# Performance work log

Hardware: AMD Instinct MI355X
Metric: run time of the kernel (lower is better)

## Reference

```python
import jax, jax.numpy as jnp
import numpy as np

B, L, D, H, HS, V, NL = 8, 513, 512, 8, 64, 513, 6  # head_size = D // H
EPS = 1e-5


def setup_inputs() -> dict:
    key = jax.random.key(0)
    ks = jax.random.split(key, 8)
    s = 0.02
    return {
        "x": jax.random.randint(ks[0], (B, L), 0, V),
        "embed": jax.random.normal(ks[1], (V, D), jnp.float32) * s,
        "pos_embed": jax.random.normal(ks[2], (L, D), jnp.float32) * s,
        "Wq": jax.random.normal(ks[3], (NL, H, D, HS), jnp.float32) * s,
        "Wk": jax.random.normal(ks[4], (NL, H, D, HS), jnp.float32) * s,
        "Wv": jax.random.normal(ks[5], (NL, H, D, HS), jnp.float32) * s,
        "ln1_g": jnp.ones((NL, D), jnp.float32),
        "ln1_b": jnp.zeros((NL, D), jnp.float32),
        "ln2_g": jnp.ones((NL, D), jnp.float32),
        "ln2_b": jnp.zeros((NL, D), jnp.float32),
        "mlp_W": jax.random.normal(ks[6], (NL, D, D), jnp.float32) * s,
        "mlp_b": jnp.zeros((NL, D), jnp.float32),
        "fc_W": jax.random.normal(ks[7], (D, V), jnp.float32) * s,
        "fc_b": jnp.zeros((V,), jnp.float32),
    }


def _layernorm(x, g, b):
    mu = jnp.mean(x, axis=-1, keepdims=True)
    var = jnp.mean(jnp.square(x - mu), axis=-1, keepdims=True)
    return (x - mu) * jax.lax.rsqrt(var + EPS) * g + b


def reference(x, embed, pos_embed, Wq, Wk, Wv, ln1_g, ln1_b, ln2_g, ln2_b,
              mlp_W, mlp_b, fc_W, fc_b):
    h = embed[x] + pos_embed[None]                       # (B, L, D)
    mask = jnp.tril(jnp.ones((L, L), bool))              # causal tril buffer
    scale = HS ** -0.5
    for i in range(NL):
        xn = _layernorm(h, ln1_g[i], ln1_b[i])
        # all heads batched (original loops per head; same math)
        q = jnp.einsum('bld,hde->bhle', xn, Wq[i])
        k = jnp.einsum('bld,hde->bhle', xn, Wk[i])
        v = jnp.einsum('bld,hde->bhle', xn, Wv[i])
        w = jnp.einsum('bhle,bhme->bhlm', q, k) * scale
        w = jnp.where(mask, w, -jnp.inf)
        w = jax.nn.softmax(w, axis=-1)
        y = jnp.einsum('bhlm,bhme->bhle', w, v)
        y = y.transpose(0, 2, 1, 3).reshape(B, L, D)     # concat heads
        h = y + h
        xn2 = _layernorm(h, ln2_g[i], ln2_b[i])
        h = jax.nn.gelu(xn2 @ mlp_W[i] + mlp_b[i], approximate=False) + h
    return h @ fc_W + fc_b                               # (B, L, V) logits
```

## Files before the change

### kernel.cpp

```cpp
#include <hip/hip_runtime.h>
#include <hip/hip_bf16.h>
#include <math.h>

#define B 8
#define L 513
#define D 512
#define H 8
#define HS 64
#define V 513
#define NL 6
#define BL (B * L)
#define LP 576
#define EPS 1e-5f

typedef __attribute__((ext_vector_type(8))) short bf16x8;
typedef __attribute__((ext_vector_type(4))) float f32x4;

__device__ inline ushort f2b(float f) {
    __hip_bfloat16 h = __float2bfloat16(f);
    return *reinterpret_cast<ushort*>(&h);
}

__device__ inline void ln_row(float4 v0, float4 v1, const float* g,
                              const float* b, int lane, ushort* orow)
{
    float s = v0.x + v0.y + v0.z + v0.w + v1.x + v1.y + v1.z + v1.w;
#pragma unroll
    for (int off = 1; off < 64; off <<= 1) s += __shfl_xor(s, off);
    const float mu = s * (1.f / D);
    float d0 = v0.x - mu, d1 = v0.y - mu, d2 = v0.z - mu, d3 = v0.w - mu;
    float d4 = v1.x - mu, d5 = v1.y - mu, d6 = v1.z - mu, d7 = v1.w - mu;
    float ss = d0*d0 + d1*d1 + d2*d2 + d3*d3 + d4*d4 + d5*d5 + d6*d6 + d7*d7;
#pragma unroll
    for (int off = 1; off < 64; off <<= 1) ss += __shfl_xor(ss, off);
    const float rs = rsqrtf(ss * (1.f / D) + EPS);
    const float* gp = g + lane * 8;
    const float* bp = b + lane * 8;
    float4 g0 = *(const float4*)gp, g1 = *(const float4*)(gp + 4);
    float4 b0 = *(const float4*)bp, b1 = *(const float4*)(bp + 4);
    ushort4 u0, u1;
    u0.x = f2b(d0 * rs * g0.x + b0.x); u0.y = f2b(d1 * rs * g0.y + b0.y);
    u0.z = f2b(d2 * rs * g0.z + b0.z); u0.w = f2b(d3 * rs * g0.w + b0.w);
    u1.x = f2b(d4 * rs * g1.x + b1.x); u1.y = f2b(d5 * rs * g1.y + b1.y);
    u1.z = f2b(d6 * rs * g1.z + b1.z); u1.w = f2b(d7 * rs * g1.w + b1.w);
    *(ushort4*)orow       = u0;
    *(ushort4*)(orow + 4) = u1;
}

__global__ __launch_bounds__(256) void ln4_k(const float* __restrict__ x,
                                             const float* __restrict__ g,
                                             const float* __restrict__ b,
                                             ushort* __restrict__ o)
{
    const int wave = threadIdx.x >> 6, lane = threadIdx.x & 63;
    const int row = blockIdx.x * 4 + wave;
    const float* xr = x + (size_t)row * D + lane * 8;
    float4 v0 = *(const float4*)xr;
    float4 v1 = *(const float4*)(xr + 4);
    ln_row(v0, v1, g, b, lane, o + (size_t)row * D + lane * 8);
}

__global__ __launch_bounds__(256) void ln_embed4_k(const int* __restrict__ xi,
                                                   const float* __restrict__ emb,
                                                   const float* __restrict__ pos,
                                                   const float* __restrict__ g,
                                                   const float* __restrict__ b,
                                                   float* __restrict__ h,
                                                   ushort* __restrict__ o)
{
    const int wave = threadIdx.x >> 6, lane = threadIdx.x & 63;
    const int row = blockIdx.x * 4 + wave;
    const int l = row % L;
    const int tok = xi[row];
    const float* er = emb + (size_t)tok * D + lane * 8;
    const float* pr = pos + (size_t)l * D + lane * 8;
    float4 e0 = *(const float4*)er, e1 = *(const float4*)(er + 4);
    float4 p0 = *(const float4*)pr, p1 = *(const float4*)(pr + 4);
    float4 v0 = make_float4(e0.x + p0.x, e0.y + p0.y, e0.z + p0.z, e0.w + p0.w);
    float4 v1 = make_float4(e1.x + p1.x, e1.y + p1.y, e1.z + p1.z, e1.w + p1.w);
    float* hr = h + (size_t)row * D + lane * 8;
    *(float4*)hr       = v0;
    *(float4*)(hr + 4) = v1;
    ln_row(v0, v1, g, b, lane, o + (size_t)row * D + lane * 8);
}

__global__ __launch_bounds__(256) void cvt_qkv_k(const float* __restrict__ Wq,
                                                 const float* __restrict__ Wk,
                                                 const float* __restrict__ Wv,
                                                 ushort* __restrict__ Wp)
{
    const int dc = blockIdx.x;
    const int i  = blockIdx.y / H, h = blockIdx.y % H;
    const int sel = blockIdx.z;
    const float* W = (sel == 0) ? Wq : (sel == 1) ? Wk : Wv;
    const float* src = W + ((size_t)i * H + h) * D * HS + (size_t)dc * 64 * HS;
    __shared__ float T[64][65];
    const int tid = threadIdx.x;
#pragma unroll
    for (int it = 0; it < 4; ++it) {
        int idx = tid + it * 256;
        int r = idx >> 4, e4 = (idx & 15) * 4;
        float4 f = *(const float4*)(src + (size_t)r * HS + e4);
        T[r][e4] = f.x; T[r][e4 + 1] = f.y; T[r][e4 + 2] = f.z; T[r][e4 + 3] = f.w;
    }
    __syncthreads();
    ushort* dst = Wp + (size_t)i * 1536 * 512 + (size_t)(sel * 512 + h * 64) * 512 + dc * 64;
#pragma unroll
    for (int it = 0; it < 4; ++it) {
        int idx = tid + it * 256;
        int e = idx >> 4, d4 = (idx & 15) * 4;
        ushort4 u;
        u.x = f2b(T[d4][e]); u.y = f2b(T[d4 + 1][e]);
        u.z = f2b(T[d4 + 2][e]); u.w = f2b(T[d4 + 3][e]);
        *(ushort4*)(dst + (size_t)e * 512 + d4) = u;
    }
}

__global__ __launch_bounds__(256) void cvt_mlp_k(const float* __restrict__ Wm,
                                                 ushort* __restrict__ Wt)
{
    const int nt = blockIdx.x, kt = blockIdx.y, i = blockIdx.z;
    const float* src = Wm + (size_t)i * D * D;
    __shared__ float T[64][65];
    const int tid = threadIdx.x;
#pragma unroll
    for (int it = 0; it < 4; ++it) {
        int idx = tid + it * 256;
        int r = idx >> 4, e4 = (idx & 15) * 4;
        float4 f = *(const float4*)(src + (size_t)(kt * 64 + r) * D + nt * 64 + e4);
        T[r][e4] = f.x; T[r][e4 + 1] = f.y; T[r][e4 + 2] = f.z; T[r][e4 + 3] = f.w;
    }
    __syncthreads();
    ushort* dst = Wt + (size_t)i * D * D + (size_t)(nt * 64) * D + kt * 64;
#pragma unroll
    for (int it = 0; it < 4; ++it) {
        int idx = tid + it * 256;
        int e = idx >> 4, k4 = (idx & 15) * 4;
        ushort4 u;
        u.x = f2b(T[k4][e]); u.y = f2b(T[k4 + 1][e]);
        u.z = f2b(T[k4 + 2][e]); u.w = f2b(T[k4 + 3][e]);
        *(ushort4*)(dst + (size_t)e * D + k4) = u;
    }
}

__global__ __launch_bounds__(256) void cvt_fc_k(const float* __restrict__ Wf,
                                                ushort* __restrict__ Wt)
{
    const int nt = blockIdx.x, kt = blockIdx.y;
    __shared__ float T[64][65];
    const int tid = threadIdx.x;
#pragma unroll
    for (int it = 0; it < 4; ++it) {
        int idx = tid + it * 256;
        int r = idx >> 4, e4 = (idx & 15) * 4;
#pragma unroll
        for (int j = 0; j < 4; ++j) {
            int n = nt * 64 + e4 + j;
            T[r][e4 + j] = (n < V) ? Wf[(size_t)(kt * 64 + r) * V + n] : 0.f;
        }
    }
    __syncthreads();
    ushort* dst = Wt + (size_t)(nt * 64) * 512 + kt * 64;
#pragma unroll
    for (int it = 0; it < 4; ++it) {
        int idx = tid + it * 256;
        int e = idx >> 4, k4 = (idx & 15) * 4;
        ushort4 u;
        u.x = f2b(T[k4][e]); u.y = f2b(T[k4 + 1][e]);
        u.z = f2b(T[k4 + 2][e]); u.w = f2b(T[k4 + 3][e]);
        *(ushort4*)(dst + (size_t)e * 512 + k4) = u;
    }
}

template <int MODE>
__global__ __launch_bounds__(256) void mgemm_k(const ushort* __restrict__ A,
                                               const ushort* __restrict__ Bt,
                                               const float* __restrict__ bias,
                                               void* __restrict__ o0,
                                               void* __restrict__ o1,
                                               void* __restrict__ o2)
{
    __shared__ ushort As[64 * 64];
    __shared__ ushort Bs[64 * 64];
    const int tid  = threadIdx.x;
    const int wave = tid >> 6, lane = tid & 63;
    const int row0 = blockIdx.y * 64;
    const int col0 = blockIdx.x * 64;
    const int wr = (wave >> 1) * 32, wc = (wave & 1) * 32;
    const int frow = lane & 15;
    const int kb   = lane >> 4;

    const int sr0 = tid >> 3, skc = tid & 7;
    const int sr1 = (tid + 256) >> 3;
    const int ss0 = (skc ^ (sr0 & 7)) * 8;
    const int ss1 = (skc ^ (sr1 & 7)) * 8;

    f32x4 acc[2][2] = {};

    for (int k0 = 0; k0 < 512; k0 += 64) {
        {
            uint4 av = make_uint4(0u, 0u, 0u, 0u);
            if (row0 + sr0 < BL)
                av = *(const uint4*)(A + (size_t)(row0 + sr0) * 512 + k0 + skc * 8);
            *(uint4*)&As[sr0 * 64 + ss0] = av;
            uint4 bv = *(const uint4*)(Bt + (size_t)(col0 + sr0) * 512 + k0 + skc * 8);
            *(uint4*)&Bs[sr0 * 64 + ss0] = bv;
            av = make_uint4(0u, 0u, 0u, 0u);
            if (row0 + sr1 < BL)
                av = *(const uint4*)(A + (size_t)(row0 + sr1) * 512 + k0 + skc * 8);
            *(uint4*)&As[sr1 * 64 + ss1] = av;
            bv = *(const uint4*)(Bt + (size_t)(col0 + sr1) * 512 + k0 + skc * 8);
            *(uint4*)&Bs[sr1 * 64 + ss1] = bv;
        }
        __syncthreads();
#pragma unroll
        for (int ks = 0; ks < 2; ++ks) {
            bf16x8 a[2], b[2];
            const int g = ks * 4 + kb;
#pragma unroll
            for (int f = 0; f < 2; ++f) {
                const int ra_ = wr + f * 16 + frow;
                a[f] = *(const bf16x8*)&As[ra_ * 64 + ((g ^ (ra_ & 7)) * 8)];
                const int rb_ = wc + f * 16 + frow;
                b[f] = *(const bf16x8*)&Bs[rb_ * 64 + ((g ^ (rb_ & 7)) * 8)];
            }
#pragma unroll
            for (int fi = 0; fi < 2; ++fi)
#pragma unroll
                for (int fj = 0; fj < 2; ++fj)
                    acc[fi][fj] = __builtin_amdgcn_mfma_f32_16x16x32_bf16(
                        a[fi], b[fj], acc[fi][fj], 0, 0, 0);
        }
        __syncthreads();
    }

    const int rbase = row0 + wr + (lane >> 4) * 4;
    const int cbase = col0 + wc + (lane & 15);
#pragma unroll
    for (int fi = 0; fi < 2; ++fi) {
#pragma unroll
        for (int fj = 0; fj < 2; ++fj) {
            const int c = cbase + fj * 16;
#pragma unroll
            for (int rg = 0; rg < 4; ++rg) {
                const int r = rbase + fi * 16 + rg;
                if (r >= BL) continue;
                float val = acc[fi][fj][rg];
                if (MODE == 0) {
                    int buf = c >> 9, cc = c & 511;
                    int b_ = r / L, l = r % L;
                    int head = cc >> 6, e = cc & 63;
                    int bh = b_ * H + head;
                    if (buf == 0)
                        ((ushort*)o0)[((size_t)bh * L + l) * HS + e] = f2b(val);
                    else if (buf == 1)
                        ((ushort*)o1)[((size_t)bh * L + l) * HS + e] = f2b(val);
                    else
                        ((ushort*)o2)[((size_t)bh * HS + e) * LP + l] = f2b(val);
                } else if (MODE == 1) {
                    float xv = val + bias[c];
                    float gl = 0.5f * xv * (1.f + erff(xv * 0.70710678118654752f));
                    ((float*)o0)[(size_t)r * D + c] = gl + ((float*)o0)[(size_t)r * D + c];
                } else if (MODE == 3) {
                    float xv = val + bias[c];
                    float gl = 0.5f * xv * (1.f + erff(xv * 0.70710678118654752f));
                    float res = ((const float*)o1)[(size_t)r * D + c];
                    ((ushort*)o0)[(size_t)r * D + c] = f2b(gl + res);
                } else {
                    if (c < V) ((float*)o0)[(size_t)r * V + c] = val + bias[c];
                }
            }
        }
    }
}

__global__ __launch_bounds__(256) void fattn_k(const ushort* __restrict__ qb,
                                               const ushort* __restrict__ kb,
                                               const ushort* __restrict__ vT,
                                               float* __restrict__ hbuf)
{
    __shared__ ushort Qs[64 * 64];
    __shared__ ushort Ks[64 * 64];
    __shared__ ushort Vs[64 * 64];
    __shared__ ushort Ps[64][72];

    const int bx  = blockIdx.x;
    const int bh  = bx / 9;
    const int qt  = 8 - (bx % 9);
    const int q0  = qt * 64;
    const int tid = threadIdx.x;
    const int wave = tid >> 6, lane = tid & 63;
    const int lg = lane >> 4, li = lane & 15;
    const int wq = wave * 16;

    const int sr0 = tid >> 3, skc = tid & 7;
    const int sr1 = (tid + 256) >> 3;
    const int ss0 = (skc ^ (sr0 & 7)) * 8;
    const int ss1 = (skc ^ (sr1 & 7)) * 8;

    {
        int qr = q0 + sr0;
        uint4 v = make_uint4(0u, 0u, 0u, 0u);
        if (qr < L) v = *(const uint4*)(qb + ((size_t)bh * L + qr) * HS + skc * 8);
        *(uint4*)&Qs[sr0 * 64 + ss0] = v;
        qr = q0 + sr1;
        v = make_uint4(0u, 0u, 0u, 0u);
        if (qr < L) v = *(const uint4*)(qb + ((size_t)bh * L + qr) * HS + skc * 8);
        *(uint4*)&Qs[sr1 * 64 + ss1] = v;
    }

    const short one_b = (short)0x3F80;
    const bf16x8 ones = { one_b, one_b, one_b, one_b, one_b, one_b, one_b, one_b };

    f32x4 accO[4] = {};
    f32x4 accL = {};

    const int n_mt = qt + 1;
    uint4 kr[2], vr[2];

    auto loadKV = [&](int t) {
        int mr = t * 64 + sr0;
        kr[0] = make_uint4(0u, 0u, 0u, 0u);
        if (mr < L) kr[0] = *(const uint4*)(kb + ((size_t)bh * L + mr) * HS + skc * 8);
        vr[0] = *(const uint4*)(vT + ((size_t)bh * HS + sr0) * LP + t * 64 + skc * 8);
        mr = t * 64 + sr1;
        kr[1] = make_uint4(0u, 0u, 0u, 0u);
        if (mr < L) kr[1] = *(const uint4*)(kb + ((size_t)bh * L + mr) * HS + skc * 8);
        vr[1] = *(const uint4*)(vT + ((size_t)bh * HS + sr1) * LP + t * 64 + skc * 8);
    };
    auto writeKV = [&]() {
        *(uint4*)&Ks[sr0 * 64 + ss0] = kr[0];
        *(uint4*)&Vs[sr0 * 64 + ss0] = vr[0];
        *(uint4*)&Ks[sr1 * 64 + ss1] = kr[1];
        *(uint4*)&Vs[sr1 * 64 + ss1] = vr[1];
    };

    loadKV(0);
    writeKV();
    __syncthreads();

    for (int t = 0; t < n_mt; ++t) {
        if (t + 1 < n_mt) loadKV(t + 1);

        f32x4 accS[4] = {};
#pragma unroll
        for (int ks = 0; ks < 2; ++ks) {
            const int g = ks * 4 + lg;
            const int ra_ = wq + li;
            bf16x8 a = *(const bf16x8*)&Qs[ra_ * 64 + ((g ^ (ra_ & 7)) * 8)];
#pragma unroll
            for (int j = 0; j < 4; ++j) {
                const int rb_ = j * 16 + li;
                bf16x8 b = *(const bf16x8*)&Ks[rb_ * 64 + ((g ^ (rb_ & 7)) * 8)];
                accS[j] = __builtin_amdgcn_mfma_f32_16x16x32_bf16(a, b, accS[j], 0, 0, 0);
            }
        }

        const int m0 = t * 64;
#pragma unroll
        for (int rg = 0; rg < 4; ++rg) {
            const int qrow = q0 + wq + lg * 4 + rg;
#pragma unroll
            for (int j = 0; j < 4; ++j) {
                int mcol = m0 + j * 16 + li;
                float p = (mcol > qrow || mcol >= L) ? 0.f : __expf(accS[j][rg] * 0.125f);
                Ps[wq + lg * 4 + rg][j * 16 + li] = f2b(p);
            }
        }

#pragma unroll
        for (int ks = 0; ks < 2; ++ks) {
            bf16x8 a = *(const bf16x8*)&Ps[wq + li][ks * 32 + lg * 8];
            accL = __builtin_amdgcn_mfma_f32_16x16x32_bf16(a, ones, accL, 0, 0, 0);
#pragma unroll
            for (int j = 0; j < 4; ++j) {
                const int g = ks * 4 + lg;
                const int rb_ = j * 16 + li;
                bf16x8 b = *(const bf16x8*)&Vs[rb_ * 64 + ((g ^ (rb_ & 7)) * 8)];
                accO[j] = __builtin_amdgcn_mfma_f32_16x16x32_bf16(a, b, accO[j], 0, 0, 0);
            }
        }
        __syncthreads();
        if (t + 1 < n_mt) {
            writeKV();
            __syncthreads();
        }
    }

    const int b_ = bh / H, hh = bh % H;
#pragma unroll
    for (int rg = 0; rg < 4; ++rg) {
        const int qrow = q0 + wq + lg * 4 + rg;
        if (qrow >= L) continue;
        const float inv = 1.f / accL[rg];
        float* dst = hbuf + ((size_t)b_ * L + qrow) * D + hh * HS;
#pragma unroll
        for (int j = 0; j < 4; ++j)
            dst[j * 16 + li] += accO[j][rg] * inv;
    }
}

extern "C" void kernel_launch(void* const* d_in, const int* in_sizes, int n_in,
                              void* d_out, int out_size, void* d_ws, size_t ws_size,
                              hipStream_t stream)
{
    const int*   x    = (const int*)d_in[0];
    const float* emb  = (const float*)d_in[1];
    const float* pos  = (const float*)d_in[2];
    const float* Wq   = (const float*)d_in[3];
    const float* Wk   = (const float*)d_in[4];
    const float* Wv   = (const float*)d_in[5];
    const float* ln1g = (const float*)d_in[6];
    const float* ln1b = (const float*)d_in[7];
    const float* ln2g = (const float*)d_in[8];
    const float* ln2b = (const float*)d_in[9];
    const float* mlpW = (const float*)d_in[10];
    const float* mlpb = (const float*)d_in[11];
    const float* fcW  = (const float*)d_in[12];
    const float* fcb  = (const float*)d_in[13];
    float* out = (float*)d_out;

    char* ws = (char*)d_ws;
    float*  h   = (float*)ws;    ws += (size_t)BL * D * 4;
    ushort* qb  = (ushort*)ws;   ws += (size_t)BL * D * 2;
    ushort* kbuf= (ushort*)ws;   ws += (size_t)BL * D * 2;
    ushort* vT  = (ushort*)ws;   ws += (size_t)B * H * HS * LP * 2;
    ushort* xnb = (ushort*)ws;   ws += (size_t)BL * D * 2;
    ushort* hb  = (ushort*)ws;   ws += (size_t)BL * D * 2;
    ushort* Wp  = (ushort*)ws;   ws += (size_t)NL * 1536 * 512 * 2;
    ushort* Wtm = (ushort*)ws;   ws += (size_t)NL * D * D * 2;
    ushort* Wtf = (ushort*)ws;   ws += (size_t)576 * 512 * 2;

    cvt_qkv_k<<<dim3(8, NL * H, 3), 256, 0, stream>>>(Wq, Wk, Wv, Wp);
    cvt_mlp_k<<<dim3(8, 8, NL), 256, 0, stream>>>(mlpW, Wtm);
    cvt_fc_k<<<dim3(9, 8), 256, 0, stream>>>(fcW, Wtf);

    for (int i = 0; i < NL; ++i) {
        if (i == 0)
            ln_embed4_k<<<BL / 4, 256, 0, stream>>>(x, emb, pos, ln1g, ln1b, h, xnb);
        else
            ln4_k<<<BL / 4, 256, 0, stream>>>(h, ln1g + i * D, ln1b + i * D, xnb);
        mgemm_k<0><<<dim3(24, 65), 256, 0, stream>>>(
            xnb, Wp + (size_t)i * 1536 * 512, nullptr, qb, kbuf, vT);
        fattn_k<<<B * H * 9, 256, 0, stream>>>(qb, kbuf, vT, h);
        ln4_k<<<BL / 4, 256, 0, stream>>>(h, ln2g + i * D, ln2b + i * D, xnb);
        if (i < NL - 1)
            mgemm_k<1><<<dim3(8, 65), 256, 0, stream>>>(
                xnb, Wtm + (size_t)i * D * D, mlpb + i * D, h, nullptr, nullptr);
        else
            mgemm_k<3><<<dim3(8, 65), 256, 0, stream>>>(
                xnb, Wtm + (size_t)i * D * D, mlpb + i * D, hb, h, nullptr);
    }
    mgemm_k<2><<<dim3(9, 65), 256, 0, stream>>>(hb, Wtf, fcb, out, nullptr, nullptr);
}
```

Before: 543.9 us.

## Fold LayerNorm into GEMMs via precomputed weight row sums and in-GEMM row stats

Removes the standalone LayerNorm kernels. The gamma scaling is folded into the bf16 weights at conversion time, along with per-column sums of gamma*W and beta*W. Each GEMM now reads the fp32 residual directly, accumulates per-row sum and sum-of-squares while staging A tiles, and applies mean/rstd correction in the epilogue. The MLP residual is ping-ponged between two buffers to avoid read/write aliasing. The trade-offs are that the GEMMs load fp32 A, doubling A traffic and repeating it across column blocks, and the single-pass variance plus bf16 rounding of the un-normalized activations may reduce accuracy.

Measured after the change: 759.5 us. 1.4x slower.

```diff
diff --git a/kernel.cpp b/kernel.cpp
--- a/kernel.cpp
+++ b/kernel.cpp
@@ -21,52 +21,17 @@
     return *reinterpret_cast<ushort*>(&h);
 }
 
-__device__ inline void ln_row(float4 v0, float4 v1, const float* g,
-                              const float* b, int lane, ushort* orow)
-{
-    float s = v0.x + v0.y + v0.z + v0.w + v1.x + v1.y + v1.z + v1.w;
-#pragma unroll
-    for (int off = 1; off < 64; off <<= 1) s += __shfl_xor(s, off);
-    const float mu = s * (1.f / D);
-    float d0 = v0.x - mu, d1 = v0.y - mu, d2 = v0.z - mu, d3 = v0.w - mu;
-    float d4 = v1.x - mu, d5 = v1.y - mu, d6 = v1.z - mu, d7 = v1.w - mu;
-    float ss = d0*d0 + d1*d1 + d2*d2 + d3*d3 + d4*d4 + d5*d5 + d6*d6 + d7*d7;
-#pragma unroll
-    for (int off = 1; off < 64; off <<= 1) ss += __shfl_xor(ss, off);
-    const float rs = rsqrtf(ss * (1.f / D) + EPS);
-    const float* gp = g + lane * 8;
-    const float* bp = b + lane * 8;
-    float4 g0 = *(const float4*)gp, g1 = *(const float4*)(gp + 4);
-    float4 b0 = *(const float4*)bp, b1 = *(const float4*)(bp + 4);
-    ushort4 u0, u1;
-    u0.x = f2b(d0 * rs * g0.x + b0.x); u0.y = f2b(d1 * rs * g0.y + b0.y);
-    u0.z = f2b(d2 * rs * g0.z + b0.z); u0.w = f2b(d3 * rs * g0.w + b0.w);
-    u1.x = f2b(d4 * rs * g1.x + b1.x); u1.y = f2b(d5 * rs * g1.y + b1.y);
-    u1.z = f2b(d6 * rs * g1.z + b1.z); u1.w = f2b(d7 * rs * g1.w + b1.w);
-    *(ushort4*)orow       = u0;
-    *(ushort4*)(orow + 4) = u1;
-}
-
-__global__ __launch_bounds__(256) void ln4_k(const float* __restrict__ x,
-                                             const float* __restrict__ g,
-                                             const float* __restrict__ b,
-                                             ushort* __restrict__ o)
-{
-    const int wave = threadIdx.x >> 6, lane = threadIdx.x & 63;
-    const int row = blockIdx.x * 4 + wave;
-    const float* xr = x + (size_t)row * D + lane * 8;
-    float4 v0 = *(const float4*)xr;
-    float4 v1 = *(const float4*)(xr + 4);
-    ln_row(v0, v1, g, b, lane, o + (size_t)row * D + lane * 8);
-}
-
-__global__ __launch_bounds__(256) void ln_embed4_k(const int* __restrict__ xi,
-                                                   const float* __restrict__ emb,
-                                                   const float* __restrict__ pos,
-                                                   const float* __restrict__ g,
-                                                   const float* __restrict__ b,
-                                                   float* __restrict__ h,
-                                                   ushort* __restrict__ o)
+__device__ inline uint4 pack8(float4 a, float4 b) {
+    union { ushort u[8]; uint4 v; } r;
+    r.u[0] = f2b(a.x); r.u[1] = f2b(a.y); r.u[2] = f2b(a.z); r.u[3] = f2b(a.w);
+    r.u[4] = f2b(b.x); r.u[5] = f2b(b.y); r.u[6] = f2b(b.z); r.u[7] = f2b(b.w);
+    return r.v;
+}
+
+__global__ __launch_bounds__(256) void embed4_k(const int* __restrict__ xi,
+                                                const float* __restrict__ emb,
+                                                const float* __restrict__ pos,
+                                                float* __restrict__ h)
 {
     const int wave = threadIdx.x >> 6, lane = threadIdx.x & 63;
     const int row = blockIdx.x * 4 + wave;
@@ -76,70 +41,132 @@
     const float* pr = pos + (size_t)l * D + lane * 8;
     float4 e0 = *(const float4*)er, e1 = *(const float4*)(er + 4);
     float4 p0 = *(const float4*)pr, p1 = *(const float4*)(pr + 4);
-    float4 v0 = make_float4(e0.x + p0.x, e0.y + p0.y, e0.z + p0.z, e0.w + p0.w);
-    float4 v1 = make_float4(e1.x + p1.x, e1.y + p1.y, e1.z + p1.z, e1.w + p1.w);
     float* hr = h + (size_t)row * D + lane * 8;
-    *(float4*)hr       = v0;
-    *(float4*)(hr + 4) = v1;
-    ln_row(v0, v1, g, b, lane, o + (size_t)row * D + lane * 8);
+    *(float4*)hr       = make_float4(e0.x + p0.x, e0.y + p0.y, e0.z + p0.z, e0.w + p0.w);
+    *(float4*)(hr + 4) = make_float4(e1.x + p1.x, e1.y + p1.y, e1.z + p1.z, e1.w + p1.w);
 }
 
 __global__ __launch_bounds__(256) void cvt_qkv_k(const float* __restrict__ Wq,
                                                  const float* __restrict__ Wk,
                                                  const float* __restrict__ Wv,
-                                                 ushort* __restrict__ Wp)
-{
-    const int dc = blockIdx.x;
-    const int i  = blockIdx.y / H, h = blockIdx.y % H;
-    const int sel = blockIdx.z;
+                                                 const float* __restrict__ g1all,
+                                                 const float* __restrict__ b1all,
+                                                 ushort* __restrict__ Wp,
+                                                 float* __restrict__ s1,
+                                                 float* __restrict__ s2)
+{
+    const int i = blockIdx.x / H, h = blockIdx.x % H;
+    const int sel = blockIdx.y;
     const float* W = (sel == 0) ? Wq : (sel == 1) ? Wk : Wv;
-    const float* src = W + ((size_t)i * H + h) * D * HS + (size_t)dc * 64 * HS;
+    const float* src = W + ((size_t)i * H + h) * D * HS;
+    const float* g1 = g1all + (size_t)i * D;
+    const float* b1 = b1all + (size_t)i * D;
+
     __shared__ float T[64][65];
+    __shared__ float sP1[16][64];
+    __shared__ float sP2[16][64];
+
     const int tid = threadIdx.x;
-#pragma unroll
-    for (int it = 0; it < 4; ++it) {
-        int idx = tid + it * 256;
-        int r = idx >> 4, e4 = (idx & 15) * 4;
-        float4 f = *(const float4*)(src + (size_t)r * HS + e4);
-        T[r][e4] = f.x; T[r][e4 + 1] = f.y; T[r][e4 + 2] = f.z; T[r][e4 + 3] = f.w;
-    }
+    const int equad = (tid & 15) * 4;
+    const int jrow  = tid >> 4;
+    float p1[4] = {0, 0, 0, 0}, p2[4] = {0, 0, 0, 0};
+
+    ushort* dst = Wp + (size_t)i * 1536 * 512 + (size_t)(sel * 512 + h * 64) * 512;
+
+    for (int dc = 0; dc < 8; ++dc) {
+#pragma unroll
+        for (int it = 0; it < 4; ++it) {
+            int r = jrow + it * 16;
+            float4 f = *(const float4*)(src + (size_t)(dc * 64 + r) * HS + equad);
+            T[r][equad] = f.x; T[r][equad + 1] = f.y;
+            T[r][equad + 2] = f.z; T[r][equad + 3] = f.w;
+            float gg = g1[dc * 64 + r], bb = b1[dc * 64 + r];
+            p1[0] += gg * f.x; p1[1] += gg * f.y; p1[2] += gg * f.z; p1[3] += gg * f.w;
+            p2[0] += bb * f.x; p2[1] += bb * f.y; p2[2] += bb * f.z; p2[3] += bb * f.w;
+        }
+        __syncthreads();
+#pragma unroll
+        for (int it = 0; it < 4; ++it) {
+            int e = jrow + it * 16;
+            int d4 = equad;
+            float4 gq = *(const float4*)(g1 + dc * 64 + d4);
+            ushort4 u;
+            u.x = f2b(T[d4][e] * gq.x);     u.y = f2b(T[d4 + 1][e] * gq.y);
+            u.z = f2b(T[d4 + 2][e] * gq.z); u.w = f2b(T[d4 + 3][e] * gq.w);
+            *(ushort4*)(dst + (size_t)e * 512 + dc * 64 + d4) = u;
+        }
+        __syncthreads();
+    }
+
+#pragma unroll
+    for (int q = 0; q < 4; ++q) { sP1[jrow][equad + q] = p1[q]; sP2[jrow][equad + q] = p2[q]; }
     __syncthreads();
-    ushort* dst = Wp + (size_t)i * 1536 * 512 + (size_t)(sel * 512 + h * 64) * 512 + dc * 64;
-#pragma unroll
-    for (int it = 0; it < 4; ++it) {
-        int idx = tid + it * 256;
-        int e = idx >> 4, d4 = (idx & 15) * 4;
-        ushort4 u;
-        u.x = f2b(T[d4][e]); u.y = f2b(T[d4 + 1][e]);
-        u.z = f2b(T[d4 + 2][e]); u.w = f2b(T[d4 + 3][e]);
-        *(ushort4*)(dst + (size_t)e * 512 + d4) = u;
+    if (tid < 64) {
+        float a1 = 0.f, a2 = 0.f;
+#pragma unroll
+        for (int j = 0; j < 16; ++j) { a1 += sP1[j][tid]; a2 += sP2[j][tid]; }
+        size_t n = (size_t)i * 1536 + sel * 512 + h * 64 + tid;
+        s1[n] = a1; s2[n] = a2;
     }
 }
 
 __global__ __launch_bounds__(256) void cvt_mlp_k(const float* __restrict__ Wm,
-                                                 ushort* __restrict__ Wt)
-{
-    const int nt = blockIdx.x, kt = blockIdx.y, i = blockIdx.z;
-    const float* src = Wm + (size_t)i * D * D;
+                                                 const float* __restrict__ g2all,
+                                                 const float* __restrict__ b2all,
+                                                 ushort* __restrict__ Wt,
+                                                 float* __restrict__ s1,
+                                                 float* __restrict__ s2)
+{
+    const int nt = blockIdx.x, i = blockIdx.y;
+    const float* src = Wm + (size_t)i * D * D + nt * 64;
+    const float* g2 = g2all + (size_t)i * D;
+    const float* b2 = b2all + (size_t)i * D;
+
     __shared__ float T[64][65];
+    __shared__ float sP1[16][64];
+    __shared__ float sP2[16][64];
+
     const int tid = threadIdx.x;
-#pragma unroll
-    for (int it = 0; it < 4; ++it) {
-        int idx = tid + it * 256;
-        int r = idx >> 4, e4 = (idx & 15) * 4;
-        float4 f = *(const float4*)(src + (size_t)(kt * 64 + r) * D + nt * 64 + e4);
-        T[r][e4] = f.x; T[r][e4 + 1] = f.y; T[r][e4 + 2] = f.z; T[r][e4 + 3] = f.w;
-    }
+    const int equad = (tid & 15) * 4;
+    const int jrow  = tid >> 4;
+    float p1[4] = {0, 0, 0, 0}, p2[4] = {0, 0, 0, 0};
+
+    ushort* dst = Wt + (size_t)i * D * D + (size_t)(nt * 64) * D;
+
+    for (int kt = 0; kt < 8; ++kt) {
+#pragma unroll
+        for (int it = 0; it < 4; ++it) {
+            int r = jrow + it * 16;
+            float4 f = *(const float4*)(src + (size_t)(kt * 64 + r) * D + equad);
+            T[r][equad] = f.x; T[r][equad + 1] = f.y;
+            T[r][equad + 2] = f.z; T[r][equad + 3] = f.w;
+            float gg = g2[kt * 64 + r], bb = b2[kt * 64 + r];
+            p1[0] += gg * f.x; p1[1] += gg * f.y; p1[2] += gg * f.z; p1[3] += gg * f.w;
+            p2[0] += bb * f.x; p2[1] += bb * f.y; p2[2] += bb * f.z; p2[3] += bb * f.w;
+        }
+        __syncthreads();
+#pragma unroll
+        for (int it = 0; it < 4; ++it) {
+            int e = jrow + it * 16;
+            int k4 = equad;
+            float4 gq = *(const float4*)(g2 + kt * 64 + k4);
+            ushort4 u;
+            u.x = f2b(T[k4][e] * gq.x);     u.y = f2b(T[k4 + 1][e] * gq.y);
+            u.z = f2b(T[k4 + 2][e] * gq.z); u.w = f2b(T[k4 + 3][e] * gq.w);
+            *(ushort4*)(dst + (size_t)e * D + kt * 64 + k4) = u;
+        }
+        __syncthreads();
+    }
+
+#pragma unroll
+    for (int q = 0; q < 4; ++q) { sP1[jrow][equad + q] = p1[q]; sP2[jrow][equad + q] = p2[q]; }
     __syncthreads();
-    ushort* dst = Wt + (size_t)i * D * D + (size_t)(nt * 64) * D + kt * 64;
-#pragma unroll
-    for (int it = 0; it < 4; ++it) {
-        int idx = tid + it * 256;
-        int e = idx >> 4, k4 = (idx & 15) * 4;
-        ushort4 u;
-        u.x = f2b(T[k4][e]); u.y = f2b(T[k4 + 1][e]);
-        u.z = f2b(T[k4 + 2][e]); u.w = f2b(T[k4 + 3][e]);
-        *(ushort4*)(dst + (size_t)e * D + k4) = u;
+    if (tid < 64) {
+        float a1 = 0.f, a2 = 0.f;
+#pragma unroll
+        for (int j = 0; j < 16; ++j) { a1 += sP1[j][tid]; a2 += sP2[j][tid]; }
+        size_t n = (size_t)i * 512 + nt * 64 + tid;
+        s1[n] = a1; s2[n] = a2;
     }
 }
 
@@ -173,15 +200,21 @@
 }
 
 template <int MODE>
-__global__ __launch_bounds__(256) void mgemm_k(const ushort* __restrict__ A,
+__global__ __launch_bounds__(256) void mgemm_k(const void* __restrict__ Av,
                                                const ushort* __restrict__ Bt,
+                                               const float* __restrict__ s1,
+                                               const float* __restrict__ s2,
                                                const float* __restrict__ bias,
                                                void* __restrict__ o0,
                                                void* __restrict__ o1,
                                                void* __restrict__ o2)
 {
+    constexpr bool LNF = (MODE != 2);
     __shared__ ushort As[64 * 64];
     __shared__ ushort Bs[64 * 64];
+    __shared__ float sMu[64];
+    __shared__ float sRs[64];
+
     const int tid  = threadIdx.x;
     const int wave = tid >> 6, lane = tid & 63;
     const int row0 = blockIdx.y * 64;
@@ -195,20 +228,45 @@
     const int ss0 = (skc ^ (sr0 & 7)) * 8;
     const int ss1 = (skc ^ (sr1 & 7)) * 8;
 
+    float st_s0 = 0.f, st_q0 = 0.f, st_s1 = 0.f, st_q1 = 0.f;
+
     f32x4 acc[2][2] = {};
 
     for (int k0 = 0; k0 < 512; k0 += 64) {
-        {
+        if constexpr (LNF) {
+            const float* hA = (const float*)Av;
+            float4 f0 = {0, 0, 0, 0}, f1 = {0, 0, 0, 0};
+            if (row0 + sr0 < BL) {
+                const float* p = hA + (size_t)(row0 + sr0) * 512 + k0 + skc * 8;
+                f0 = ((const float4*)p)[0]; f1 = ((const float4*)p)[1];
+            }
+            st_s0 += f0.x + f0.y + f0.z + f0.w + f1.x + f1.y + f1.z + f1.w;
+            st_q0 += f0.x*f0.x + f0.y*f0.y + f0.z*f0.z + f0.w*f0.w
+                   + f1.x*f1.x + f1.y*f1.y + f1.z*f1.z + f1.w*f1.w;
+            *(uint4*)&As[sr0 * 64 + ss0] = pack8(f0, f1);
+            float4 g0 = {0, 0, 0, 0}, g1 = {0, 0, 0, 0};
+            if (row0 + sr1 < BL) {
+                const float* p = hA + (size_t)(row0 + sr1) * 512 + k0 + skc * 8;
+                g0 = ((const float4*)p)[0]; g1 = ((const float4*)p)[1];
+            }
+            st_s1 += g0.x + g0.y + g0.z + g0.w + g1.x + g1.y + g1.z + g1.w;
+            st_q1 += g0.x*g0.x + g0.y*g0.y + g0.z*g0.z + g0.w*g0.w
+                   + g1.x*g1.x + g1.y*g1.y + g1.z*g1.z + g1.w*g1.w;
+            *(uint4*)&As[sr1 * 64 + ss1] = pack8(g0, g1);
+        } else {
+            const ushort* A = (const ushort*)Av;
             uint4 av = make_uint4(0u, 0u, 0u, 0u);
             if (row0 + sr0 < BL)
                 av = *(const uint4*)(A + (size_t)(row0 + sr0) * 512 + k0 + skc * 8);
             *(uint4*)&As[sr0 * 64 + ss0] = av;
-            uint4 bv = *(const uint4*)(Bt + (size_t)(col0 + sr0) * 512 + k0 + skc * 8);
-            *(uint4*)&Bs[sr0 * 64 + ss0] = bv;
             av = make_uint4(0u, 0u, 0u, 0u);
             if (row0 + sr1 < BL)
                 av = *(const uint4*)(A + (size_t)(row0 + sr1) * 512 + k0 + skc * 8);
             *(uint4*)&As[sr1 * 64 + ss1] = av;
+        }
+        {
+            uint4 bv = *(const uint4*)(Bt + (size_t)(col0 + sr0) * 512 + k0 + skc * 8);
+            *(uint4*)&Bs[sr0 * 64 + ss0] = bv;
             bv = *(const uint4*)(Bt + (size_t)(col0 + sr1) * 512 + k0 + skc * 8);
             *(uint4*)&Bs[sr1 * 64 + ss1] = bv;
         }
@@ -234,6 +292,21 @@
         __syncthreads();
     }
 
+    if constexpr (LNF) {
+#pragma unroll
+        for (int off = 1; off < 8; off <<= 1) {
+            st_s0 += __shfl_xor(st_s0, off); st_q0 += __shfl_xor(st_q0, off);
+            st_s1 += __shfl_xor(st_s1, off); st_q1 += __shfl_xor(st_q1, off);
+        }
+        if (skc == 0) {
+            float mu0 = st_s0 * (1.f / 512);
+            sMu[sr0] = mu0; sRs[sr0] = rsqrtf(st_q0 * (1.f / 512) - mu0 * mu0 + EPS);
+            float mu1 = st_s1 * (1.f / 512);
+            sMu[sr1] = mu1; sRs[sr1] = rsqrtf(st_q1 * (1.f / 512) - mu1 * mu1 + EPS);
+        }
+        __syncthreads();
+    }
+
     const int rbase = row0 + wr + (lane >> 4) * 4;
     const int cbase = col0 + wc + (lane & 15);
 #pragma unroll
@@ -241,11 +314,17 @@
 #pragma unroll
         for (int fj = 0; fj < 2; ++fj) {
             const int c = cbase + fj * 16;
+            float s1c = 0.f, s2c = 0.f;
+            if constexpr (LNF) { s1c = s1[c]; s2c = s2[c]; }
 #pragma unroll
             for (int rg = 0; rg < 4; ++rg) {
                 const int r = rbase + fi * 16 + rg;
                 if (r >= BL) continue;
                 float val = acc[fi][fj][rg];
+                if constexpr (LNF) {
+                    const int rl = wr + (lane >> 4) * 4 + fi * 16 + rg;
+                    val = sRs[rl] * (val - sMu[rl] * s1c) + s2c;
+                }
                 if (MODE == 0) {
                     int buf = c >> 9, cc = c & 511;
                     int b_ = r / L, l = r % L;
@@ -260,7 +339,7 @@
                 } else if (MODE == 1) {
                     float xv = val + bias[c];
                     float gl = 0.5f * xv * (1.f + erff(xv * 0.70710678118654752f));
-                    ((float*)o0)[(size_t)r * D + c] = gl + ((float*)o0)[(size_t)r * D + c];
+                    ((float*)o0)[(size_t)r * D + c] = gl + ((const float*)o1)[(size_t)r * D + c];
                 } else if (MODE == 3) {
                     float xv = val + bias[c];
                     float gl = 0.5f * xv * (1.f + erff(xv * 0.70710678118654752f));
@@ -422,34 +501,43 @@
 
     char* ws = (char*)d_ws;
     float*  h   = (float*)ws;    ws += (size_t)BL * D * 4;
+    float*  h2  = (float*)ws;    ws += (size_t)BL * D * 4;
     ushort* qb  = (ushort*)ws;   ws += (size_t)BL * D * 2;
     ushort* kbuf= (ushort*)ws;   ws += (size_t)BL * D * 2;
     ushort* vT  = (ushort*)ws;   ws += (size_t)B * H * HS * LP * 2;
-    ushort* xnb = (ushort*)ws;   ws += (size_t)BL * D * 2;
     ushort* hb  = (ushort*)ws;   ws += (size_t)BL * D * 2;
     ushort* Wp  = (ushort*)ws;   ws += (size_t)NL * 1536 * 512 * 2;
     ushort* Wtm = (ushort*)ws;   ws += (size_t)NL * D * D * 2;
     ushort* Wtf = (ushort*)ws;   ws += (size_t)576 * 512 * 2;
-
-    cvt_qkv_k<<<dim3(8, NL * H, 3), 256, 0, stream>>>(Wq, Wk, Wv, Wp);
-    cvt_mlp_k<<<dim3(8, 8, NL), 256, 0, stream>>>(mlpW, Wtm);
+    float* s1q  = (float*)ws;    ws += (size_t)NL * 1536 * 4;
+    float* s2q  = (float*)ws;    ws += (size_t)NL * 1536 * 4;
+    float* s1m  = (float*)ws;    ws += (size_t)NL * 512 * 4;
+    float* s2m  = (float*)ws;    ws += (size_t)NL * 512 * 4;
+
+    cvt_qkv_k<<<dim3(NL * H, 3), 256, 0, stream>>>(Wq, Wk, Wv, ln1g, ln1b, Wp, s1q, s2q);
+    cvt_mlp_k<<<dim3(8, NL), 256, 0, stream>>>(mlpW, ln2g, ln2b, Wtm, s1m, s2m);
     cvt_fc_k<<<dim3(9, 8), 256, 0, stream>>>(fcW, Wtf);
 
+    embed4_k<<<BL / 4, 256, 0, stream>>>(x, emb, pos, h);
+
+    float* hc = h;
+    float* hn = h2;
     for (int i = 0; i < NL; ++i) {
-        if (i == 0)
-            ln_embed4_k<<<BL / 4, 256, 0, stream>>>(x, emb, pos, ln1g, ln1b, h, xnb);
-        else
-            ln4_k<<<BL / 4, 256, 0, stream>>>(h, ln1g + i * D, ln1b + i * D, xnb);
         mgemm_k<0><<<dim3(24, 65), 256, 0, stream>>>(
-            xnb, Wp + (size_t)i * 1536 * 512, nullptr, qb, kbuf, vT);
-        fattn_k<<<B * H * 9, 256, 0, stream>>>(qb, kbuf, vT, h);
-        ln4_k<<<BL / 4, 256, 0, stream>>>(h, ln2g + i * D, ln2b + i * D, xnb);
-        if (i < NL - 1)
+            hc, Wp + (size_t)i * 1536 * 512, s1q + (size_t)i * 1536, s2q + (size_t)i * 1536,
+            nullptr, qb, kbuf, vT);
+        fattn_k<<<B * H * 9, 256, 0, stream>>>(qb, kbuf, vT, hc);
+        if (i < NL - 1) {
             mgemm_k<1><<<dim3(8, 65), 256, 0, stream>>>(
-                xnb, Wtm + (size_t)i * D * D, mlpb + i * D, h, nullptr, nullptr);
-        else
+                hc, Wtm + (size_t)i * D * D, s1m + (size_t)i * 512, s2m + (size_t)i * 512,
+                mlpb + i * D, hn, hc, nullptr);
+            float* t = hc; hc = hn; hn = t;
+        } else {
             mgemm_k<3><<<dim3(8, 65), 256, 0, stream>>>(
-                xnb, Wtm + (size_t)i * D * D, mlpb + i * D, hb, h, nullptr);
-    }
-    mgemm_k<2><<<dim3(9, 65), 256, 0, stream>>>(hb, Wtf, fcb, out, nullptr, nullptr);
-}
+                hc, Wtm + (size_t)i * D * D, s1m + (size_t)i * 512, s2m + (size_t)i * 512,
+                mlpb + i * D, hb, hc, nullptr);
+        }
+    }
+    mgemm_k<2><<<dim3(9, 65), 256, 0, stream>>>(hb, Wtf, nullptr, nullptr, fcb,
+                                                out, nullptr, nullptr);
+}
```
